# Performance work log

Measured on AMD Instinct MI355X. Metric: run time of the kernel, lower is better.

Reference implementation:

```python
import jax, jax.numpy as jnp
import numpy as np

# ---- static configuration (from init_kwargs) ----
L = 36.0            # cubic cell edge (bohr)
G = 180             # grid points per axis
NA = 64             # number of atoms
NRAD = 8            # basis['n']
NL = 4              # basis['l']
RO = 2.5            # basis['r_o'] (bohr)
A = L / G           # grid spacing (orthorhombic -> U = diag(A))
RMAX = int(np.ceil(RO / A))          # half-width of periodic box (13)
B = 2 * RMAX + 1                     # box edge (27)
VCELL = A ** 3                       # |det U|
# static coefficient mask: keep (n,l,m) with |m - NL| <= l  (same as tril*flip(tril))
_MASK = np.abs(np.arange(2 * NL + 1)[None, :] - NL) <= np.arange(NL)[:, None]


def _make_W():
    # orthonormalization matrix W = S^{-1/2} for radials phi_n(r) = r^2 (r_o - r)^{n+2}
    r = np.linspace(0.0, RO, 4000)
    phi = np.stack([r ** 2 * (RO - r) ** (n + 2) for n in range(NRAD)])
    S = np.trapz(phi[:, None] * phi[None, :], r, axis=-1)
    w, v = np.linalg.eigh(S)
    return (v @ np.diag(w ** -0.5) @ v.T).astype(np.float32)


def setup_inputs() -> dict:
    key = jax.random.key(0)
    k1, k2 = jax.random.split(key)
    rho = jax.random.uniform(k1, (G, G, G), dtype=jnp.float32)       # electron density >= 0
    positions = jax.random.uniform(k2, (NA, 3), dtype=jnp.float32) * L
    return {"rho": rho, "positions": positions, "W": jnp.asarray(_make_W())}


def _sph_padded(theta, phi):
    # real spherical harmonics, zero-padded to [NL, 2*NL+1, ...] with m at index NL+m
    ct = jnp.cos(theta); st = jnp.sin(theta)
    cp = jnp.cos(phi); sp = jnp.sin(phi)
    c2p = jnp.cos(2 * phi); s2p = jnp.sin(2 * phi)
    c3p = jnp.cos(3 * phi); s3p = jnp.sin(3 * phi)
    z = jnp.zeros_like(theta)
    one = jnp.ones_like(theta)
    Y = {
        (0, 0): 0.28209479177387814 * one,
        (1, -1): 0.4886025119029199 * st * sp,
        (1, 0): 0.4886025119029199 * ct,
        (1, 1): 0.4886025119029199 * st * cp,
        (2, -2): 0.5462742152960396 * st ** 2 * s2p,
        (2, -1): 1.0925484305920792 * st * ct * sp,
        (2, 0): 0.31539156525252005 * (3 * ct ** 2 - 1),
        (2, 1): 1.0925484305920792 * st * ct * cp,
        (2, 2): 0.5462742152960396 * st ** 2 * c2p,
        (3, -3): 0.5900435899266435 * st ** 3 * s3p,
        (3, -2): 1.445305721320277 * st ** 2 * ct * s2p,
        (3, -1): 0.4570457994644658 * st * (5 * ct ** 2 - 1) * sp,
        (3, 0): 0.3731763325901154 * (5 * ct ** 3 - 3 * ct),
        (3, 1): 0.4570457994644658 * st * (5 * ct ** 2 - 1) * cp,
        (3, 2): 1.445305721320277 * st ** 2 * ct * c2p,
        (3, 3): 0.5900435899266435 * st ** 3 * c3p,
    }
    rows = []
    for l in range(NL):
        pad = [z] * (NL - l)
        rows.append(jnp.stack(pad + [Y[(l, m)] for m in range(-l, l + 1)] + pad))
    return jnp.stack(rows)  # [NL, 2NL+1, B, B, B]


def _project_atom(rho, pos, W):
    a = jnp.float32(A)
    cm = jnp.round(pos / a)            # nearest grid index of atom (U_inv @ pos)
    dr = pos - a * cm                  # sub-grid displacement
    offs = jnp.arange(-RMAX, RMAX + 1, dtype=jnp.float32)
    # periodic mesh indices (box_around / fmod wrap)
    Xm = jnp.mod(offs + cm[0], G).astype(jnp.int32)
    Ym = jnp.mod(offs + cm[1], G).astype(jnp.int32)
    Zm = jnp.mod(offs + cm[2], G).astype(jnp.int32)
    srho = rho[Xm[:, None, None], Ym[None, :, None], Zm[None, None, :]]  # [B,B,B] gather
    # euclidean coords relative to the atom
    Xs = (offs * a - dr[0])[:, None, None]
    Ys = (offs * a - dr[1])[None, :, None]
    Zs = (offs * a - dr[2])[None, None, :]
    Xs, Ys, Zs = jnp.broadcast_arrays(Xs, Ys, Zs)
    R = jnp.sqrt(Xs ** 2 + Ys ** 2 + Zs ** 2)
    Rsafe = jnp.where(R < 1e-12, 1.0, R)
    Theta = jnp.where(R < 1e-12, 0.0, jnp.arccos(jnp.clip(Zs / Rsafe, -1.0, 1.0)))
    Phi = jnp.arctan2(Ys, Xs)
    angs = _sph_padded(Theta, Phi)                       # [NL, 2NL+1, B,B,B]
    ns = jnp.arange(NRAD, dtype=jnp.float32)[:, None, None, None]
    phi_n = jnp.where(R < RO, R ** 2 * jnp.maximum(RO - R, 0.0) ** (ns + 2.0), 0.0)
    rads = jnp.einsum('nm,mijk->nijk', W, phi_n) * jnp.float32(VCELL)  # [NRAD, B,B,B]
    coeff = jnp.einsum('lmijk,nijk,ijk->nlm', angs, rads, srho)        # [NRAD, NL, 2NL+1]
    return coeff[:, _MASK].reshape(-1)                    # [NRAD * NL^2] = 128


def reference(rho, positions, W):
    # vmap over atoms (single species -> identical box shape per atom)
    return jax.vmap(lambda p: _project_atom(rho, p, W))(positions)  # [NA, 128]
```

## Files before the change

### kernel.cpp

```cpp
#include <hip/hip_runtime.h>

#define G 180
#define NRAD 8
#define RO_F 2.5f
#define A_F 0.2f
#define VCELL_F 0.008f
#define CELLS 19683
#define SLABS 8
#define NATOMS 64


__global__ __launch_bounds__(256, 2) void proj_kernel(
    const float* __restrict__ rho, const float* __restrict__ pos,
    float* __restrict__ ws)
{
    const int atom = blockIdx.y;
    const int slab = blockIdx.x;
    const int tid  = threadIdx.x;
    const int lane = tid & 63;
    const int waveid = tid >> 6;

    const float px = pos[atom*3+0], py = pos[atom*3+1], pz = pos[atom*3+2];
    const float cmx = rintf(px * 5.0f), cmy = rintf(py * 5.0f), cmz = rintf(pz * 5.0f);
    const float drx = px - A_F*cmx, dry = py - A_F*cmy, drz = pz - A_F*cmz;
    const int icx = (int)cmx - 13, icy = (int)cmy - 13, icz = (int)cmz - 13;

    float acc[128];
    #pragma unroll
    for (int j = 0; j < 128; ++j) acc[j] = 0.0f;

    for (int c = slab*256 + tid; c < CELLS; c += SLABS*256) {
        int i = c / 729;
        int rem = c - i*729;
        int j = rem / 27;
        int k = rem - j*27;
        int gx = i + icx; gx += (gx < 0) ? G : 0; gx -= (gx >= G) ? G : 0;
        int gy = j + icy; gy += (gy < 0) ? G : 0; gy -= (gy >= G) ? G : 0;
        int gz = k + icz; gz += (gz < 0) ? G : 0; gz -= (gz >= G) ? G : 0;
        float s = rho[(gx*G + gy)*G + gz];

        float x = (float)(i-13)*A_F - drx;
        float y = (float)(j-13)*A_F - dry;
        float z = (float)(k-13)*A_F - drz;
        float r2 = x*x + y*y + z*z;
        float inv = rsqrtf(fmaxf(r2, 1e-24f));
        float R = r2 * inv;
        if (R < RO_F) {
            float t = RO_F - R;
            float ux = x*inv, uy = y*inv, uz = z*inv;
            float uz2 = uz*uz;
            float ux2 = ux*ux, uy2 = uy*uy;
            float ys[16];
            ys[0]  = 0.28209479177f * s;
            ys[1]  = 0.48860251190f * uy * s;
            ys[2]  = 0.48860251190f * uz * s;
            ys[3]  = 0.48860251190f * ux * s;
            ys[4]  = 1.09254843059f * ux*uy * s;
            ys[5]  = 1.09254843059f * uy*uz * s;
            ys[6]  = 0.31539156525f * (3.0f*uz2 - 1.0f) * s;
            ys[7]  = 1.09254843059f * ux*uz * s;
            ys[8]  = 0.54627421530f * (ux2 - uy2) * s;
            ys[9]  = 0.59004358993f * uy*(3.0f*ux2 - uy2) * s;
            ys[10] = 2.89061144264f * ux*uy*uz * s;
            ys[11] = 0.45704579946f * uy*(5.0f*uz2 - 1.0f) * s;
            ys[12] = 0.37317633259f * uz*(5.0f*uz2 - 3.0f) * s;
            ys[13] = 0.45704579946f * ux*(5.0f*uz2 - 1.0f) * s;
            ys[14] = 1.44530572132f * (ux2 - uy2)*uz * s;
            ys[15] = 0.59004358993f * ux*(ux2 - 3.0f*uy2) * s;

            float p = r2 * t * t;
            #pragma unroll
            for (int n = 0; n < NRAD; ++n) {
                #pragma unroll
                for (int q = 0; q < 16; ++q)
                    acc[n*16+q] = fmaf(p, ys[q], acc[n*16+q]);
                p *= t;
            }
        }
    }

    __shared__ float red[4][64][33];
    __shared__ float stage[4][8][32];
    const int col  = lane & 31;
    const int half = lane >> 5;
    #pragma unroll
    for (int cb = 0; cb < 4; ++cb) {
        __syncthreads();
        #pragma unroll
        for (int q = 0; q < 32; ++q)
            red[waveid][lane][q] = acc[cb*32 + q];
        __syncthreads();
        float csum = 0.0f;
        #pragma unroll
        for (int r = 0; r < 32; ++r)
            csum += red[waveid][half*32 + r][col];
        stage[cb][waveid*2 + half][col] = csum;
    }
    __syncthreads();
    if (tid < 128) {
        const int cb = tid >> 5, c2 = tid & 31;
        float sum = 0.0f;
        #pragma unroll
        for (int r = 0; r < 8; ++r)
            sum += stage[cb][r][c2];
        ws[(atom*SLABS + slab)*128 + tid] = sum;
    }
}

__global__ void finalize_kernel(const float* __restrict__ ws,
                                const float* __restrict__ W,
                                float* __restrict__ out)
{
    const int atom = blockIdx.x;
    const int t = threadIdx.x;
    const int n = t >> 4, q = t & 15;
    const float* base = ws + atom*SLABS*128;
    float red[8];
    #pragma unroll
    for (int k = 0; k < 8; ++k) {
        float sk = 0.0f;
        #pragma unroll
        for (int s = 0; s < 8; ++s)
            sk += base[s*128 + k*16 + q];
        red[k] = sk;
    }
    float sum = 0.0f;
    #pragma unroll
    for (int k = 0; k < 8; ++k)
        sum = fmaf(W[n*8+k], red[k], sum);
    out[atom*128 + t] = sum * VCELL_F;
}

extern "C" void kernel_launch(void* const* d_in, const int* in_sizes, int n_in,
                              void* d_out, int out_size, void* d_ws, size_t ws_size,
                              hipStream_t stream) {
    const float* rho = (const float*)d_in[0];
    const float* pos = (const float*)d_in[1];
    const float* W   = (const float*)d_in[2];
    float* out = (float*)d_out;
    float* ws  = (float*)d_ws;

    dim3 grid(SLABS, NATOMS);
    proj_kernel<<<grid, 256, 0, stream>>>(rho, pos, ws);
    finalize_kernel<<<NATOMS, 128, 0, stream>>>(ws, W, out);
}
```

Baseline: 78.00 us.

## Split radial accumulators across two block halves to cut registers and raise occupancy

```diff
diff --git a/kernel.cpp b/kernel.cpp
--- a/kernel.cpp
+++ b/kernel.cpp
@@ -1,7 +1,6 @@
 #include <hip/hip_runtime.h>
 
 #define G 180
-#define NRAD 8
 #define RO_F 2.5f
 #define A_F 0.2f
 #define VCELL_F 0.008f
@@ -10,12 +9,13 @@
 #define NATOMS 64
 
 
-__global__ __launch_bounds__(256, 2) void proj_kernel(
+__global__ __launch_bounds__(256, 4) void proj_kernel(
     const float* __restrict__ rho, const float* __restrict__ pos,
     float* __restrict__ ws)
 {
     const int atom = blockIdx.y;
-    const int slab = blockIdx.x;
+    const int slab = blockIdx.x & (SLABS - 1);
+    const int nh   = blockIdx.x >> 3;
     const int tid  = threadIdx.x;
     const int lane = tid & 63;
     const int waveid = tid >> 6;
@@ -25,9 +25,9 @@
     const float drx = px - A_F*cmx, dry = py - A_F*cmy, drz = pz - A_F*cmz;
     const int icx = (int)cmx - 13, icy = (int)cmy - 13, icz = (int)cmz - 13;
 
-    float acc[128];
+    float acc[64];
     #pragma unroll
-    for (int j = 0; j < 128; ++j) acc[j] = 0.0f;
+    for (int j = 0; j < 64; ++j) acc[j] = 0.0f;
 
     for (int c = slab*256 + tid; c < CELLS; c += SLABS*256) {
         int i = c / 729;
@@ -47,44 +47,47 @@
         float R = r2 * inv;
         if (R < RO_F) {
             float t = RO_F - R;
+            float t2 = t * t;
+            float pb = r2 * t2 * s;
+            if (nh) pb *= t2 * t2;
+            float p0 = pb, p1 = pb*t, p2 = p1*t, p3 = p2*t;
+
             float ux = x*inv, uy = y*inv, uz = z*inv;
-            float uz2 = uz*uz;
-            float ux2 = ux*ux, uy2 = uy*uy;
-            float ys[16];
-            ys[0]  = 0.28209479177f * s;
-            ys[1]  = 0.48860251190f * uy * s;
-            ys[2]  = 0.48860251190f * uz * s;
-            ys[3]  = 0.48860251190f * ux * s;
-            ys[4]  = 1.09254843059f * ux*uy * s;
-            ys[5]  = 1.09254843059f * uy*uz * s;
-            ys[6]  = 0.31539156525f * (3.0f*uz2 - 1.0f) * s;
-            ys[7]  = 1.09254843059f * ux*uz * s;
-            ys[8]  = 0.54627421530f * (ux2 - uy2) * s;
-            ys[9]  = 0.59004358993f * uy*(3.0f*ux2 - uy2) * s;
-            ys[10] = 2.89061144264f * ux*uy*uz * s;
-            ys[11] = 0.45704579946f * uy*(5.0f*uz2 - 1.0f) * s;
-            ys[12] = 0.37317633259f * uz*(5.0f*uz2 - 3.0f) * s;
-            ys[13] = 0.45704579946f * ux*(5.0f*uz2 - 1.0f) * s;
-            ys[14] = 1.44530572132f * (ux2 - uy2)*uz * s;
-            ys[15] = 0.59004358993f * ux*(ux2 - 3.0f*uy2) * s;
+            float ux2 = ux*ux, uy2 = uy*uy, uz2 = uz*uz;
+            float xy = ux*uy, yz = uy*uz, xz = ux*uz;
 
-            float p = r2 * t * t;
-            #pragma unroll
-            for (int n = 0; n < NRAD; ++n) {
-                #pragma unroll
-                for (int q = 0; q < 16; ++q)
-                    acc[n*16+q] = fmaf(p, ys[q], acc[n*16+q]);
-                p *= t;
-            }
+            #define ACC4(Q, Y) { float yv = (Y); \
+                acc[Q]      = fmaf(p0, yv, acc[Q]); \
+                acc[16 + Q] = fmaf(p1, yv, acc[16 + Q]); \
+                acc[32 + Q] = fmaf(p2, yv, acc[32 + Q]); \
+                acc[48 + Q] = fmaf(p3, yv, acc[48 + Q]); }
+
+            ACC4(0,  0.28209479177f);
+            ACC4(1,  0.48860251190f * uy);
+            ACC4(2,  0.48860251190f * uz);
+            ACC4(3,  0.48860251190f * ux);
+            ACC4(4,  1.09254843059f * xy);
+            ACC4(5,  1.09254843059f * yz);
+            ACC4(6,  0.31539156525f * (3.0f*uz2 - 1.0f));
+            ACC4(7,  1.09254843059f * xz);
+            ACC4(8,  0.54627421530f * (ux2 - uy2));
+            ACC4(9,  0.59004358993f * uy*(3.0f*ux2 - uy2));
+            ACC4(10, 2.89061144264f * xy*uz);
+            ACC4(11, 0.45704579946f * uy*(5.0f*uz2 - 1.0f));
+            ACC4(12, 0.37317633259f * uz*(5.0f*uz2 - 3.0f));
+            ACC4(13, 0.45704579946f * ux*(5.0f*uz2 - 1.0f));
+            ACC4(14, 1.44530572132f * (ux2 - uy2)*uz);
+            ACC4(15, 0.59004358993f * ux*(ux2 - 3.0f*uy2));
+            #undef ACC4
         }
     }
 
     __shared__ float red[4][64][33];
-    __shared__ float stage[4][8][32];
+    __shared__ float stage[2][8][32];
     const int col  = lane & 31;
     const int half = lane >> 5;
     #pragma unroll
-    for (int cb = 0; cb < 4; ++cb) {
+    for (int cb = 0; cb < 2; ++cb) {
         __syncthreads();
         #pragma unroll
         for (int q = 0; q < 32; ++q)
@@ -97,13 +100,13 @@
         stage[cb][waveid*2 + half][col] = csum;
     }
     __syncthreads();
-    if (tid < 128) {
+    if (tid < 64) {
         const int cb = tid >> 5, c2 = tid & 31;
         float sum = 0.0f;
         #pragma unroll
         for (int r = 0; r < 8; ++r)
             sum += stage[cb][r][c2];
-        ws[(atom*SLABS + slab)*128 + tid] = sum;
+        ws[((atom*2 + nh)*SLABS + slab)*64 + tid] = sum;
     }
 }
 
@@ -114,14 +117,15 @@
     const int atom = blockIdx.x;
     const int t = threadIdx.x;
     const int n = t >> 4, q = t & 15;
-    const float* base = ws + atom*SLABS*128;
+    const float* base = ws + atom*2*SLABS*64;
     float red[8];
     #pragma unroll
     for (int k = 0; k < 8; ++k) {
+        const float* hb = base + (k >> 2)*SLABS*64 + (k & 3)*16 + q;
         float sk = 0.0f;
         #pragma unroll
         for (int s = 0; s < 8; ++s)
-            sk += base[s*128 + k*16 + q];
+            sk += hb[s*64];
         red[k] = sk;
     }
     float sum = 0.0f;
@@ -140,7 +144,7 @@
     float* out = (float*)d_out;
     float* ws  = (float*)d_ws;
 
-    dim3 grid(SLABS, NATOMS);
+    dim3 grid(SLABS*2, NATOMS);
     proj_kernel<<<grid, 256, 0, stream>>>(rho, pos, ws);
     finalize_kernel<<<NATOMS, 128, 0, stream>>>(ws, W, out);
 }
```

Result: no change. 79.56 us (+2.0%).
